# Performance work log

Hardware: AMD Instinct MI355X
Metric: run time of the kernel (lower is better)

## Reference

```python
import jax, jax.numpy as jnp
import numpy as np

SINKHORN_ITERS = 20
EPS = 1e-6


def setup_inputs() -> dict:
    key = jax.random.key(0)
    k1, k2 = jax.random.split(key)
    x = jax.random.normal(k1, (4, 4096, 4096), dtype=jnp.float32)
    W = jax.random.normal(k2, (4096, 4096), dtype=jnp.float32) * 0.02
    return {"x": x, "W": W}


def _sinkhorn(W):
    # W: [N, N] logits -> doubly-stochastic (Birkhoff) matrix, unit marginals
    P = jnp.exp(W)

    def body(_, P):
        P = P * (1.0 / (P.sum(axis=-2, keepdims=True) + EPS))  # column normalize
        P = P * (1.0 / (P.sum(axis=-1, keepdims=True) + EPS))  # row normalize
        return P

    return jax.lax.fori_loop(0, SINKHORN_ITERS, body, P)


def reference(x, W):
    W_proj = _sinkhorn(W)          # [N, N]
    out = jnp.matmul(x, W_proj)    # [B, S, N] @ [N, N] -> [B, S, N]
    return out
```

## Files before the change

### kernel.cpp

```cpp
#include <hip/hip_runtime.h>
#include <hip/hip_bf16.h>
#include <cstdint>
#include <cstddef>

#define NN 4096
#define SINK_ITERS 20
#define EPSV 1e-6f

typedef unsigned short u16;
typedef __attribute__((ext_vector_type(8))) short bf16x8;
typedef __attribute__((ext_vector_type(4))) short bf16x4;
typedef __attribute__((ext_vector_type(4))) float f32x4;

__device__ __forceinline__ float bf2f(u16 u) {
  union { unsigned int i; float f; } x; x.i = ((unsigned int)u) << 16; return x.f;
}
__device__ __forceinline__ u16 f2bf(float f) {
  union { float f; unsigned int i; } x; x.f = f;
  unsigned int i = x.i;
  unsigned int r = i + 0x7FFFu + ((i >> 16) & 1u);
  return (u16)(r >> 16);
}

typedef const __attribute__((address_space(1))) unsigned int* gas_p;
typedef __attribute__((address_space(3))) unsigned int* las_p;
__device__ __forceinline__ void gload16(const void* g, void* l) {
  __builtin_amdgcn_global_load_lds((gas_p)g, (las_p)l, 16, 0, 0);
}

__device__ __forceinline__ void gstore(float* p, float v) {
  __hip_atomic_store(p, v, __ATOMIC_RELAXED, __HIP_MEMORY_SCOPE_AGENT);
}
__device__ __forceinline__ float gloadc(const float* p) {
  return __hip_atomic_load(p, __ATOMIC_RELAXED, __HIP_MEMORY_SCOPE_AGENT);
}


#define SINK_WGS 256
#define SINK_SMEM (131072 + 1024 + 1024 + 8192)

__device__ __forceinline__ void gsyncF(unsigned* grp, int me, unsigned goal) {
  __syncthreads();
  int t = threadIdx.x;
  if (t < 64) {
    if (t == 0)
      __hip_atomic_store(grp + me, goal, __ATOMIC_RELAXED, __HIP_MEMORY_SCOPE_AGENT);
    unsigned v;
    long spin = 0;
    do {
      v = (t < 16) ? __hip_atomic_load(grp + t, __ATOMIC_RELAXED, __HIP_MEMORY_SCOPE_AGENT)
                   : goal;
    } while (__any(v < goal) && ++spin < 500000000L);
  }
  asm volatile("" ::: "memory");
  __syncthreads();
}

__global__ __launch_bounds__(512) void k_sinkhorn(
    const float* __restrict__ W, u16* __restrict__ Pt,
    float* __restrict__ Spart, float* __restrict__ Tpart, unsigned* bar) {
  extern __shared__ char smem[];
  u16* Kt = (u16*)smem;
  float* u_loc = (float*)(smem + 131072);
  float* v_loc = u_loc + 256;
  float* red = v_loc + 256;

  int wg = blockIdx.x;
  int a = wg >> 4, b = wg & 15;
  int i0 = a * 256, j0 = b * 256;
  int t = threadIdx.x;
  int lane = t & 63, wv = t >> 6;
  int cg = t & 31;

  unsigned* colbar = bar + b * 16;
  unsigned* rowbar = bar + (16 + a) * 16;

#pragma unroll
  for (int k = 0; k < 32; ++k) {
    int q = t + 512 * k;
    int il = q >> 6;
    int jc = (q & 63) << 2;
    f32x4 wvv = *(const f32x4*)(W + (size_t)(i0 + il) * NN + (j0 + jc));
    bf16x4 r;
#pragma unroll
    for (int c = 0; c < 4; ++c) r[c] = (short)f2bf(expf(wvv[c]));
    *(bf16x4*)(Kt + il * 256 + jc) = r;
  }
  if (t < 256) { u_loc[t] = 1.f; v_loc[t] = 1.f; }
  __syncthreads();

  for (int it = 0; it < SINK_ITERS; ++it) {
    int par = (it & 1) * 16;
    if (t < 256 && it > 0) {
      int pb = ((it - 1) & 1) * 16;
      float Ts = 0.f;
#pragma unroll
      for (int p = 0; p < 16; ++p) Ts += gloadc(&Tpart[(pb + p) * NN + i0 + t]);
      float ul = u_loc[t];
      u_loc[t] = ul / (ul * Ts + EPSV);
    }
    __syncthreads();

    float acc[8] = {0.f, 0.f, 0.f, 0.f, 0.f, 0.f, 0.f, 0.f};
#pragma unroll
    for (int k = 0; k < 16; ++k) {
      int row = (t >> 5) + 16 * k;
      bf16x8 kv = *(const bf16x8*)(Kt + row * 256 + cg * 8);
      float ui = u_loc[row];
#pragma unroll
      for (int c = 0; c < 8; ++c) acc[c] += ui * bf2f((u16)kv[c]);
    }
#pragma unroll
    for (int c = 0; c < 8; ++c) acc[c] += __shfl_xor(acc[c], 32, 64);
    if (lane < 32) {
#pragma unroll
      for (int c = 0; c < 8; ++c) red[wv * 256 + cg * 8 + c] = acc[c];
    }
    __syncthreads();
    if (t < 256) {
      float s = 0.f;
#pragma unroll
      for (int w = 0; w < 8; ++w) s += red[w * 256 + t];
      gstore(&Spart[(par + a) * NN + j0 + t], s);
    }
    gsyncF(colbar, a, (unsigned)(it + 1));

    if (t < 256) {
      float Ss = 0.f;
#pragma unroll
      for (int p = 0; p < 16; ++p) Ss += gloadc(&Spart[(par + p) * NN + j0 + t]);
      float vo = v_loc[t];
      v_loc[t] = vo / (vo * Ss + EPSV);
    }
    __syncthreads();

    f32x4 va = *(const f32x4*)(v_loc + cg * 8);
    f32x4 vb2 = *(const f32x4*)(v_loc + cg * 8 + 4);
    float tr[16];
#pragma unroll
    for (int k = 0; k < 16; ++k) {
      int row = (t >> 5) + 16 * k;
      bf16x8 kv = *(const bf16x8*)(Kt + row * 256 + cg * 8);
      float s = 0.f;
#pragma unroll
      for (int c = 0; c < 4; ++c) s += bf2f((u16)kv[c]) * va[c];
#pragma unroll
      for (int c = 0; c < 4; ++c) s += bf2f((u16)kv[4 + c]) * vb2[c];
      tr[k] = s;
    }
#pragma unroll
    for (int k = 0; k < 16; ++k) {
#pragma unroll
      for (int d = 1; d <= 16; d <<= 1) tr[k] += __shfl_xor(tr[k], d, 64);
    }
    if (lane == 0 || lane == 32) {
#pragma unroll
      for (int k = 0; k < 16; ++k) red[(t >> 5) + 16 * k] = tr[k];
    }
    __syncthreads();
    if (t < 256) gstore(&Tpart[(par + b) * NN + i0 + t], red[t]);
    gsyncF(rowbar, b, (unsigned)(it + 1));
  }

  if (t < 256) {
    int pb = ((SINK_ITERS - 1) & 1) * 16;
    float Ts = 0.f;
#pragma unroll
    for (int p = 0; p < 16; ++p) Ts += gloadc(&Tpart[(pb + p) * NN + i0 + t]);
    float ul = u_loc[t];
    u_loc[t] = ul / (ul * Ts + EPSV);
  }
  __syncthreads();

  {
    int jl = t & 255, h = t >> 8;
    float vv = v_loc[jl];
    size_t prow = (size_t)(j0 + jl) * NN + i0;
#pragma unroll
    for (int g = 0; g < 16; ++g) {
      int gg = h * 16 + g;
      int il0 = gg * 8;
      bf16x8 r;
#pragma unroll
      for (int e = 0; e < 8; ++e)
        r[e] = (short)f2bf(u_loc[il0 + e] * bf2f(Kt[(il0 + e) * 256 + jl]) * vv);
      *(bf16x8*)(Pt + prow + gg * 8) = r;
    }
  }
}

__global__ void k_f2bf(const float* __restrict__ X, u16* __restrict__ Xb, long n8) {
  long stride = (long)gridDim.x * blockDim.x;
  for (long i = (long)blockIdx.x * blockDim.x + threadIdx.x; i < n8; i += stride) {
    long idx = i * 8;
    f32x4 a = *(const f32x4*)(X + idx);
    f32x4 b = *(const f32x4*)(X + idx + 4);
    bf16x8 r;
#pragma unroll
    for (int c = 0; c < 4; ++c) r[c] = (short)f2bf(a[c]);
#pragma unroll
    for (int c = 0; c < 4; ++c) r[4 + c] = (short)f2bf(b[c]);
    *(bf16x8*)(Xb + idx) = r;
  }
}

#define GBM 256
#define GBN 256
#define GBK 64
#define GNT (NN / GBK)
#define GEMM_SMEM 131072

__global__ __launch_bounds__(512, 2) void k_gemm256(const u16* __restrict__ A,
                                                    const u16* __restrict__ Bt,
                                                    float* __restrict__ C) {
  extern __shared__ __align__(1024) char gsm[];

  int bid = blockIdx.x;
  int xcd = bid & 7, sidx = bid >> 3;
  int bm = (xcd << 3) | (sidx >> 4);
  int bn = sidx & 15;
  size_t m0 = (size_t)bm * GBM, n0 = (size_t)bn * GBN;

  int tid = threadIdx.x;
  int lane = tid & 63, w = tid >> 6;
  int wm = w >> 2, wn = w & 3;
  int l15 = lane & 15, kgb = (lane >> 4) * 16;
  int xk = kgb ^ (((l15 >> 3) & 1) << 5);

  int aoff[8], boff[4];
#pragma unroll
  for (int m = 0; m < 8; ++m) aoff[m] = (m * 16 + l15) * 64 + xk;
#pragma unroll
  for (int n = 0; n < 4; ++n) boff[n] = ((wn & 1) * 64 + n * 16 + l15) * 64 + xk;

  int dst2[2], sA[2][2], sB[2][2];
#pragma unroll
  for (int i = 0; i < 2; ++i) {
    int d = (i * 512 + tid) * 16;
    int L = d ^ (((d >> 9) & 1) << 5);
    int ks = L >> 13, r = (L >> 6) & 127, cb = L & 63;
    int kelem = ks * 32 + (cb >> 1);
    dst2[i] = d;
#pragma unroll
    for (int h = 0; h < 2; ++h) {
      sA[h][i] = (int)((m0 + h * 128 + r) * NN) + kelem;
      sB[h][i] = (int)((n0 + h * 128 + r) * NN) + kelem;
    }
  }

  f32x4 acc[8][4];
#pragma unroll
  for (int m = 0; m < 8; ++m)
#pragma unroll
    for (int n = 0; n < 4; ++n) acc[m][n] = (f32x4){0.f, 0.f, 0.f, 0.f};

#define STAGE_ALL(CUR, K0)                                                        \
  {                                                                               \
    char* base_ = gsm + (CUR) * 65536;                                            \
    _Pragma("unroll") for (int h_ = 0; h_ < 2; ++h_)                              \
      _Pragma("unroll") for (int i_ = 0; i_ < 2; ++i_)                            \
        gload16(A + (size_t)(sA[h_][i_] + (K0)), base_ + h_ * 16384 + dst2[i_]);  \
    _Pragma("unroll") for (int h_ = 0; h_ < 2; ++h_)                              \
      _Pragma("unroll") for (int i_ = 0; i_ < 2; ++i_)                            \
        gload16(Bt + (size_t)(sB[h_][i_] + (K0)), base_ + 32768 + h_ * 16384 + dst2[i_]); \
  }

  STAGE_ALL(0, 0)
  STAGE_ALL(1, GBK)

  for (int t = 0; t < GNT; ++t) {
    int cur = t & 1;
    if (t < GNT - 1) {
      asm volatile("s_waitcnt vmcnt(8)" ::: "memory");
    } else {
      asm volatile("s_waitcnt vmcnt(0)" ::: "memory");
    }
    __builtin_amdgcn_sched_barrier(0);
    __builtin_amdgcn_s_barrier();
    __builtin_amdgcn_sched_barrier(0);

    const char* Ab = gsm + cur * 65536 + wm * 16384;
    const char* Bb = gsm + cur * 65536 + 32768 + (wn >> 1) * 16384;

    bf16x8 af[4][2], bfr[4][2];

#pragma unroll
    for (int m = 0; m < 4; ++m)
#pragma unroll
      for (int ks = 0; ks < 2; ++ks) af[m][ks] = *(const bf16x8*)(Ab + ks * 8192 + aoff[m]);
#pragma unroll
    for (int n = 0; n < 2; ++n)
#pragma unroll
      for (int ks = 0; ks < 2; ++ks) bfr[n][ks] = *(const bf16x8*)(Bb + ks * 8192 + boff[n]);
    __builtin_amdgcn_s_setprio(1);
#pragma unroll
    for (int m = 0; m < 4; ++m)
#pragma unroll
      for (int n = 0; n < 2; ++n)
#pragma unroll
        for (int ks = 0; ks < 2; ++ks)
          acc[m][n] = __builtin_amdgcn_mfma_f32_16x16x32_bf16(af[m][ks], bfr[n][ks], acc[m][n], 0, 0, 0);
    __builtin_amdgcn_s_setprio(0);

#pragma unroll
    for (int n = 2; n < 4; ++n)
#pragma unroll
      for (int ks = 0; ks < 2; ++ks) bfr[n][ks] = *(const bf16x8*)(Bb + ks * 8192 + boff[n]);
    __builtin_amdgcn_s_setprio(1);
#pragma unroll
    for (int m = 0; m < 4; ++m)
#pragma unroll
      for (int n = 2; n < 4; ++n)
#pragma unroll
        for (int ks = 0; ks < 2; ++ks)
          acc[m][n] = __builtin_amdgcn_mfma_f32_16x16x32_bf16(af[m][ks], bfr[n][ks], acc[m][n], 0, 0, 0);
    __builtin_amdgcn_s_setprio(0);

#pragma unroll
    for (int m = 0; m < 4; ++m)
#pragma unroll
      for (int ks = 0; ks < 2; ++ks) af[m][ks] = *(const bf16x8*)(Ab + ks * 8192 + aoff[m + 4]);
    __builtin_amdgcn_s_setprio(1);
#pragma unroll
    for (int m = 0; m < 4; ++m)
#pragma unroll
      for (int n = 2; n < 4; ++n)
#pragma unroll
        for (int ks = 0; ks < 2; ++ks)
          acc[4 + m][n] = __builtin_amdgcn_mfma_f32_16x16x32_bf16(af[m][ks], bfr[n][ks], acc[4 + m][n], 0, 0, 0);
    __builtin_amdgcn_s_setprio(0);

    asm volatile("s_waitcnt lgkmcnt(0)" ::: "memory");
    __builtin_amdgcn_sched_barrier(0);
    __builtin_amdgcn_s_barrier();
    __builtin_amdgcn_sched_barrier(0);
    if (t + 2 < GNT) STAGE_ALL(cur, (t + 2) * GBK)

    __builtin_amdgcn_s_setprio(1);
#pragma unroll
    for (int m = 0; m < 4; ++m)
#pragma unroll
      for (int n = 0; n < 2; ++n)
#pragma unroll
        for (int ks = 0; ks < 2; ++ks)
          acc[4 + m][n] = __builtin_amdgcn_mfma_f32_16x16x32_bf16(af[m][ks], bfr[n][ks], acc[4 + m][n], 0, 0, 0);
    __builtin_amdgcn_s_setprio(0);
  }
#undef STAGE_ALL

#pragma unroll
  for (int m = 0; m < 8; ++m) {
    size_t gr = m0 + (size_t)wm * 128 + m * 16 + (lane >> 4) * 4;
#pragma unroll
    for (int n = 0; n < 4; ++n) {
      size_t gc = n0 + (size_t)wn * 64 + n * 16 + l15;
#pragma unroll
      for (int i = 0; i < 4; ++i)
        C[(gr + i) * NN + gc] = acc[m][n][i];
    }
  }
}

#define BM 128
#define BN 128
#define BK 32
#define NT (NN / BK)

__global__ __launch_bounds__(256) void k_gemm(const u16* __restrict__ A,
                                              const u16* __restrict__ Bt,
                                              float* __restrict__ C) {
  __shared__ __align__(16) u16 lA[2][BM * BK];
  __shared__ __align__(16) u16 lB[2][BN * BK];

  int bid = blockIdx.x;
  int swz = (bid & 7) * 512 + (bid >> 3);
  int bm = swz >> 5, bn = swz & 31;

  int tid = threadIdx.x;
  int lane = tid & 63, w = tid >> 6;
  int wm = (w >> 1) * 64, wn = (w & 1) * 64;
  size_t m0 = (size_t)bm * BM, n0 = (size_t)bn * BN;

  f32x4 acc[4][4];
#pragma unroll
  for (int a = 0; a < 4; ++a)
#pragma unroll
    for (int b = 0; b < 4; ++b) acc[a][b] = (f32x4){0.f, 0.f, 0.f, 0.f};

  int srow = tid >> 2;
  int skc = (tid & 3) * 8;

  auto stage = [&](int buf, int t) {
    int k0 = t * BK;
#pragma unroll
    for (int it = 0; it < 2; ++it) {
      int row = it * 64 + srow;
      gload16(A + (m0 + row) * NN + k0 + skc, &lA[buf][row * BK + skc]);
      gload16(Bt + (n0 + row) * NN + k0 + skc, &lB[buf][row * BK + skc]);
    }
  };

  stage(0, 0);
  __syncthreads();

  int arow = wm + (lane & 15);
  int brow = wn + (lane & 15);
  int kc = (lane >> 4) * 8;

  for (int t = 0; t < NT; ++t) {
    int cur = t & 1;
    if (t < NT - 1) stage(cur ^ 1, t + 1);
    bf16x8 af[4], bfr[4];
#pragma unroll
    for (int f = 0; f < 4; ++f) {
      af[f] = *(const bf16x8*)&lA[cur][(arow + f * 16) * BK + kc];
      bfr[f] = *(const bf16x8*)&lB[cur][(brow + f * 16) * BK + kc];
    }
#pragma unroll
    for (int fm = 0; fm < 4; ++fm)
#pragma unroll
      for (int fn = 0; fn < 4; ++fn)
        acc[fm][fn] = __builtin_amdgcn_mfma_f32_16x16x32_bf16(af[fm], bfr[fn], acc[fm][fn], 0, 0, 0);
    __syncthreads();
  }

#pragma unroll
  for (int fm = 0; fm < 4; ++fm) {
    int r0 = wm + fm * 16 + (lane >> 4) * 4;
#pragma unroll
    for (int fn = 0; fn < 4; ++fn) {
      int c0 = wn + fn * 16 + (lane & 15);
#pragma unroll
      for (int i = 0; i < 4; ++i) {
        C[(m0 + r0 + i) * NN + n0 + c0] = acc[fm][fn][i];
      }
    }
  }
}

extern "C" void kernel_launch(void* const* d_in, const int* in_sizes, int n_in,
                              void* d_out, int out_size, void* d_ws, size_t ws_size,
                              hipStream_t stream) {
  const float* x = (const float*)d_in[0];
  const float* W = (const float*)d_in[1];
  float* out = (float*)d_out;

  char* ws = (char*)d_ws;
  const size_t XB_OFF = 0;
  const size_t PT_OFF = 134217728;
  const size_t SC_OFF = 167772160;
  if (ws_size < SC_OFF + (66 * (size_t)NN) * sizeof(float)) return;

  u16* xb = (u16*)(ws + XB_OFF);
  u16* Ptb = (u16*)(ws + PT_OFF);

  float* Sp = (float*)(ws + SC_OFF);
  float* Tp = Sp + 32 * NN;
  unsigned* bar = (unsigned*)(Tp + 32 * NN);

  k_f2bf<<<2048, 256, 0, stream>>>(x, xb, (long)out_size / 8);

  bool coop = true;
  int dev = 0;
  hipDeviceProp_t prop;
  if (hipGetDevice(&dev) != hipSuccess) coop = false;
  else if (hipGetDeviceProperties(&prop, dev) != hipSuccess) coop = false;
  else if (prop.multiProcessorCount < SINK_WGS) coop = false;
  if (coop && hipFuncSetAttribute((const void*)k_sinkhorn,
                                  hipFuncAttributeMaxDynamicSharedMemorySize,
                                  SINK_SMEM) != hipSuccess)
    coop = false;
  if (!coop) return;

  hipMemsetAsync(bar, 0, 32 * 16 * sizeof(unsigned), stream);
  k_sinkhorn<<<SINK_WGS, 512, SINK_SMEM, stream>>>(W, Ptb, Sp, Tp, bar);

  bool big = (hipFuncSetAttribute((const void*)k_gemm256,
                                  hipFuncAttributeMaxDynamicSharedMemorySize,
                                  GEMM_SMEM) == hipSuccess);
  if (big) {
    k_gemm256<<<1024, 512, GEMM_SMEM, stream>>>(xb, Ptb, out);
    if (hipGetLastError() != hipSuccess) big = false;
  }
  if (!big) k_gemm<<<4096, 256, 0, stream>>>(xb, Ptb, out);
}
```

Baseline: 803.4 us.

## Restructure GEMM main loop into 8-phase ping-pong schedule with interleaved staging

Rewrites the bf16 GEMM K-loop to unroll two K-tiles per iteration. Global-to-LDS loads for the next tile are split into quarter-sized chunks and issued between the four MFMA phases, with barriers around each phase. This interleaves memory traffic with matrix math at a finer grain, aiming to hide load latency. In exchange it adds more workgroup barriers per tile and makes the buffer-reuse ordering more fragile.

```diff
diff --git a/kernel.cpp b/kernel.cpp
--- a/kernel.cpp
+++ b/kernel.cpp
@@ -34,7 +34,6 @@
 __device__ __forceinline__ float gloadc(const float* p) {
   return __hip_atomic_load(p, __ATOMIC_RELAXED, __HIP_MEMORY_SCOPE_AGENT);
 }
-
 
 #define SINK_WGS 256
 #define SINK_SMEM (131072 + 1024 + 1024 + 8192)
@@ -208,6 +207,7 @@
 #define GBN 256
 #define GBK 64
 #define GNT (NN / GBK)
+#define GNT2 (GNT / 2)
 #define GEMM_SMEM 131072
 
 __global__ __launch_bounds__(512, 2) void k_gemm256(const u16* __restrict__ A,
@@ -254,99 +254,112 @@
 #pragma unroll
     for (int n = 0; n < 4; ++n) acc[m][n] = (f32x4){0.f, 0.f, 0.f, 0.f};
 
-#define STAGE_ALL(CUR, K0)                                                        \
-  {                                                                               \
-    char* base_ = gsm + (CUR) * 65536;                                            \
-    _Pragma("unroll") for (int h_ = 0; h_ < 2; ++h_)                              \
-      _Pragma("unroll") for (int i_ = 0; i_ < 2; ++i_)                            \
-        gload16(A + (size_t)(sA[h_][i_] + (K0)), base_ + h_ * 16384 + dst2[i_]);  \
-    _Pragma("unroll") for (int h_ = 0; h_ < 2; ++h_)                              \
-      _Pragma("unroll") for (int i_ = 0; i_ < 2; ++i_)                            \
-        gload16(Bt + (size_t)(sB[h_][i_] + (K0)), base_ + 32768 + h_ * 16384 + dst2[i_]); \
-  }
-
-  STAGE_ALL(0, 0)
-  STAGE_ALL(1, GBK)
-
-  for (int t = 0; t < GNT; ++t) {
-    int cur = t & 1;
-    if (t < GNT - 1) {
-      asm volatile("s_waitcnt vmcnt(8)" ::: "memory");
-    } else {
-      asm volatile("s_waitcnt vmcnt(0)" ::: "memory");
-    }
-    __builtin_amdgcn_sched_barrier(0);
-    __builtin_amdgcn_s_barrier();
-    __builtin_amdgcn_sched_barrier(0);
-
-    const char* Ab = gsm + cur * 65536 + wm * 16384;
-    const char* Bb = gsm + cur * 65536 + 32768 + (wn >> 1) * 16384;
-
-    bf16x8 af[4][2], bfr[4][2];
-
-#pragma unroll
-    for (int m = 0; m < 4; ++m)
-#pragma unroll
-      for (int ks = 0; ks < 2; ++ks) af[m][ks] = *(const bf16x8*)(Ab + ks * 8192 + aoff[m]);
-#pragma unroll
-    for (int n = 0; n < 2; ++n)
-#pragma unroll
-      for (int ks = 0; ks < 2; ++ks) bfr[n][ks] = *(const bf16x8*)(Bb + ks * 8192 + boff[n]);
-    __builtin_amdgcn_s_setprio(1);
-#pragma unroll
-    for (int m = 0; m < 4; ++m)
-#pragma unroll
-      for (int n = 0; n < 2; ++n)
-#pragma unroll
-        for (int ks = 0; ks < 2; ++ks)
-          acc[m][n] = __builtin_amdgcn_mfma_f32_16x16x32_bf16(af[m][ks], bfr[n][ks], acc[m][n], 0, 0, 0);
-    __builtin_amdgcn_s_setprio(0);
-
-#pragma unroll
-    for (int n = 2; n < 4; ++n)
-#pragma unroll
-      for (int ks = 0; ks < 2; ++ks) bfr[n][ks] = *(const bf16x8*)(Bb + ks * 8192 + boff[n]);
-    __builtin_amdgcn_s_setprio(1);
-#pragma unroll
-    for (int m = 0; m < 4; ++m)
-#pragma unroll
-      for (int n = 2; n < 4; ++n)
-#pragma unroll
-        for (int ks = 0; ks < 2; ++ks)
-          acc[m][n] = __builtin_amdgcn_mfma_f32_16x16x32_bf16(af[m][ks], bfr[n][ks], acc[m][n], 0, 0, 0);
-    __builtin_amdgcn_s_setprio(0);
-
-#pragma unroll
-    for (int m = 0; m < 4; ++m)
-#pragma unroll
-      for (int ks = 0; ks < 2; ++ks) af[m][ks] = *(const bf16x8*)(Ab + ks * 8192 + aoff[m + 4]);
-    __builtin_amdgcn_s_setprio(1);
-#pragma unroll
-    for (int m = 0; m < 4; ++m)
-#pragma unroll
-      for (int n = 2; n < 4; ++n)
-#pragma unroll
-        for (int ks = 0; ks < 2; ++ks)
-          acc[4 + m][n] = __builtin_amdgcn_mfma_f32_16x16x32_bf16(af[m][ks], bfr[n][ks], acc[4 + m][n], 0, 0, 0);
-    __builtin_amdgcn_s_setprio(0);
-
-    asm volatile("s_waitcnt lgkmcnt(0)" ::: "memory");
-    __builtin_amdgcn_sched_barrier(0);
-    __builtin_amdgcn_s_barrier();
-    __builtin_amdgcn_sched_barrier(0);
-    if (t + 2 < GNT) STAGE_ALL(cur, (t + 2) * GBK)
-
-    __builtin_amdgcn_s_setprio(1);
-#pragma unroll
-    for (int m = 0; m < 4; ++m)
-#pragma unroll
-      for (int n = 0; n < 2; ++n)
-#pragma unroll
-        for (int ks = 0; ks < 2; ++ks)
-          acc[4 + m][n] = __builtin_amdgcn_mfma_f32_16x16x32_bf16(af[m][ks], bfr[n][ks], acc[4 + m][n], 0, 0, 0);
-    __builtin_amdgcn_s_setprio(0);
-  }
-#undef STAGE_ALL
+#define ST_A(D, H, KT)                                                       \
+  { char* b_ = gsm + (D) * 65536 + (H) * 16384;                              \
+    gload16(A + (size_t)(sA[H][0] + (KT) * GBK), b_ + dst2[0]);              \
+    gload16(A + (size_t)(sA[H][1] + (KT) * GBK), b_ + dst2[1]); }
+#define ST_B(D, H, KT)                                                       \
+  { char* b_ = gsm + (D) * 65536 + 32768 + (H) * 16384;                      \
+    gload16(Bt + (size_t)(sB[H][0] + (KT) * GBK), b_ + dst2[0]);             \
+    gload16(Bt + (size_t)(sB[H][1] + (KT) * GBK), b_ + dst2[1]); }
+
+#define RD_A(BASE, M0)                                                       \
+  _Pragma("unroll") for (int m = 0; m < 4; ++m)                              \
+  _Pragma("unroll") for (int ks = 0; ks < 2; ++ks)                           \
+      af[m][ks] = *(const bf16x8*)((BASE) + ks * 8192 + aoff[(M0) + m]);
+#define RD_B(BASE, N0)                                                       \
+  _Pragma("unroll") for (int n = 0; n < 2; ++n)                              \
+  _Pragma("unroll") for (int ks = 0; ks < 2; ++ks)                           \
+      bfr[(N0) + n][ks] = *(const bf16x8*)((BASE) + ks * 8192 + boff[(N0) + n]);
+#define MM(AM, AN)                                                           \
+  __builtin_amdgcn_s_setprio(1);                                             \
+  _Pragma("unroll") for (int m = 0; m < 4; ++m)                              \
+  _Pragma("unroll") for (int n = 0; n < 2; ++n)                              \
+  _Pragma("unroll") for (int ks = 0; ks < 2; ++ks)                           \
+      acc[(AM) + m][(AN) + n] = __builtin_amdgcn_mfma_f32_16x16x32_bf16(     \
+          af[m][ks], bfr[(AN) + n][ks], acc[(AM) + m][(AN) + n], 0, 0, 0);   \
+  __builtin_amdgcn_s_setprio(0);
+#define BAR __builtin_amdgcn_s_barrier()
+#define LGKM0 asm volatile("s_waitcnt lgkmcnt(0)" ::: "memory")
+
+  ST_A(0, 0, 0) ST_A(0, 1, 0) ST_B(0, 0, 0) ST_B(0, 1, 0)
+  ST_B(1, 0, 1) ST_B(1, 1, 1)
+  asm volatile("s_waitcnt vmcnt(4)" ::: "memory");
+  BAR;
+
+  for (int t2 = 0; t2 < GNT2; ++t2) {
+    bool pf = (t2 < GNT2 - 1);
+    int k1 = 2 * t2 + 1, k2 = 2 * t2 + 2, k3 = 2 * t2 + 3;
+
+    {
+      const char* Ab = gsm + wm * 16384;
+      const char* Bb = gsm + 32768 + (wn >> 1) * 16384;
+      bf16x8 af[4][2], bfr[4][2];
+
+      RD_A(Ab, 0) RD_B(Bb, 0)
+      ST_A(1, 0, k1)
+      asm volatile("s_waitcnt lgkmcnt(8)" ::: "memory");
+      BAR; LGKM0;
+      MM(0, 0)
+      BAR;
+
+      RD_B(Bb, 2)
+      ST_A(1, 1, k1)
+      BAR; LGKM0;
+      MM(0, 2)
+      BAR;
+
+      RD_A(Ab, 4)
+      if (pf) ST_B(0, 0, k2)
+      BAR; LGKM0;
+      MM(4, 2)
+      BAR;
+
+      if (pf) ST_B(0, 1, k2)
+      MM(4, 0)
+      if (pf) { asm volatile("s_waitcnt vmcnt(4)" ::: "memory"); }
+      else    { asm volatile("s_waitcnt vmcnt(0)" ::: "memory"); }
+      BAR;
+    }
+
+    {
+      const char* Ab = gsm + 65536 + wm * 16384;
+      const char* Bb = gsm + 65536 + 32768 + (wn >> 1) * 16384;
+      bf16x8 af[4][2], bfr[4][2];
+
+      RD_A(Ab, 0) RD_B(Bb, 0)
+      if (pf) ST_A(0, 0, k2)
+      asm volatile("s_waitcnt lgkmcnt(8)" ::: "memory");
+      BAR; LGKM0;
+      MM(0, 0)
+      BAR;
+
+      RD_B(Bb, 2)
+      if (pf) ST_A(0, 1, k2)
+      BAR; LGKM0;
+      MM(0, 2)
+      BAR;
+
+      RD_A(Ab, 4)
+      if (pf) ST_B(1, 0, k3)
+      BAR; LGKM0;
+      MM(4, 2)
+      BAR;
+
+      if (pf) ST_B(1, 1, k3)
+      MM(4, 0)
+      if (pf) { asm volatile("s_waitcnt vmcnt(4)" ::: "memory"); }
+      else    { asm volatile("s_waitcnt vmcnt(0)" ::: "memory"); }
+      BAR;
+    }
+  }
+#undef ST_A
+#undef ST_B
+#undef RD_A
+#undef RD_B
+#undef MM
+#undef BAR
+#undef LGKM0
 
 #pragma unroll
   for (int m = 0; m < 8; ++m) {
```

New measurement: 707.6 us. 11.9% less time.
